# Performance work log

Measured on AMD Instinct MI355X. Metric: run time of the kernel, lower is better.

Reference implementation:

```python
import jax, jax.numpy as jnp
import numpy as np

C = 256
H = 4  # hard-coded head count in SA_Layer reshapes
EPS = 1e-5


def _bn(x, gamma, beta):
    # training-mode BatchNorm1d over (batch, length) per channel; x: [b,c,n]
    m = jnp.mean(x, axis=(0, 2), keepdims=True)
    v = jnp.var(x, axis=(0, 2), keepdims=True)
    return gamma[None, :, None] * (x - m) * jax.lax.rsqrt(v + EPS) + beta[None, :, None]


def _conv1(w, x, b=None):
    # 1x1 Conv1d == per-point matmul; w: [o,c], x: [b,c,n]
    y = jnp.einsum('oc,bcn->bon', w, x)
    return y if b is None else y + b[None, :, None]


def _sa_layer(x, xyz_emb, qk_w, v_w, v_b, t_w, t_b, bn_g, bn_b):
    b, c, n = x.shape
    h = x + xyz_emb                      # [b,c,n]
    q = _conv1(qk_w, h)                  # [b,c,n]  (q and k share weights)
    # quirky reshape: permute to [b,n,c] then view as [b,H,n,c//H]
    x_q = jnp.transpose(q, (0, 2, 1)).reshape(b, H, n, c // H)
    x_k = q.reshape(b, H, c // H, n)     # standard channel head split
    x_v = _conv1(v_w, h, v_b).reshape(b, H, c // H, n)
    energy = jnp.matmul(x_q, x_k)        # [b,H,n,n]
    att = jax.nn.softmax(energy, axis=-1)
    att = jax.nn.softmax(att, axis=-2)   # dual softmax
    x_r = jnp.matmul(x_v, att).reshape(b, c, n)
    x_r = jax.nn.relu(_bn(_conv1(t_w, x - x_r, t_b), bn_g, bn_b))
    return x + x_r


def setup_inputs() -> dict:
    key = jax.random.key(0)
    ks = jax.random.split(key, 16)
    B, N = 4, 2048
    s = 1.0 / np.sqrt(C)
    inp = {
        'x': jax.random.normal(ks[0], (B, C, N), jnp.float32),
        'xyz': jax.random.normal(ks[1], (B, N, 3), jnp.float32),
        'conv1_w': jax.random.normal(ks[2], (C, C), jnp.float32) * s,
        'pos_w': jax.random.normal(ks[3], (C, 3), jnp.float32) * 0.5,
        'pos_b': jax.random.normal(ks[4], (C,), jnp.float32) * 0.02,
        'bn1_g': jnp.ones((C,), jnp.float32),
        'bn1_b': jnp.zeros((C,), jnp.float32),
        'qk_w': jax.random.normal(ks[5], (4, C, C), jnp.float32) * s,
        'v_w': jax.random.normal(ks[6], (4, C, C), jnp.float32) * s,
        'v_b': jax.random.normal(ks[7], (4, C), jnp.float32) * 0.02,
        't_w': jax.random.normal(ks[8], (4, C, C), jnp.float32) * s,
        't_b': jax.random.normal(ks[9], (4, C), jnp.float32) * 0.02,
        'bn_g': jnp.ones((4, C), jnp.float32),
        'bn_b': jnp.zeros((4, C), jnp.float32),
    }
    return inp


def reference(x, xyz, conv1_w, pos_w, pos_b, bn1_g, bn1_b,
              qk_w, v_w, v_b, t_w, t_b, bn_g, bn_b):
    # xyz: [B,N,3] -> permute -> pos_xyz (1x1 conv)
    xyz_emb = jnp.einsum('oi,bni->bon', pos_w, xyz) + pos_b[None, :, None]  # [b,C,n]
    h = jax.nn.relu(_bn(_conv1(conv1_w, x), bn1_g, bn1_b))
    outs = []
    for i in range(4):
        h = _sa_layer(h, xyz_emb, qk_w[i], v_w[i], v_b[i],
                      t_w[i], t_b[i], bn_g[i], bn_b[i])
        outs.append(h)
    return jnp.concatenate(outs, axis=1)  # [b, 4*C, n]
```

## Files before the change

### kernel.cpp

```cpp
#include <hip/hip_runtime.h>
#include <math.h>

#define Bsz 4
#define Cch 256
#define Npt 2048
#define Hh  4
#define NL  4
#define BN_CNT (Bsz * Npt)
#define EPSV 1e-5f
#define NROW (16 * Npt)
#define L2E 1.44269504f

typedef _Float16 f16x8 __attribute__((ext_vector_type(8)));
typedef _Float16 f16x4 __attribute__((ext_vector_type(4)));
typedef float    f32x4 __attribute__((ext_vector_type(4)));

__device__ __forceinline__ float fexp2(float x) { return __builtin_amdgcn_exp2f(x); }

__device__ __forceinline__ void gld16(const _Float16* g, _Float16* l) {
    __builtin_amdgcn_global_load_lds(
        (const __attribute__((address_space(1))) unsigned int*)g,
        (__attribute__((address_space(3))) unsigned int*)l, 16, 0, 0);
}

__global__ void k_xyz_emb(const float* __restrict__ xyz, const float* __restrict__ pw,
                          const float* __restrict__ pb, float* __restrict__ emb) {
    int idx = blockIdx.x * 256 + threadIdx.x;
    int n = idx & (Npt - 1);
    int c = (idx >> 11) & (Cch - 1);
    int b = idx >> 19;
    const float* xz = xyz + (b * Npt + n) * 3;
    emb[idx] = pw[c * 3 + 0] * xz[0] + pw[c * 3 + 1] * xz[1] + pw[c * 3 + 2] * xz[2] + pb[c];
}

__global__ void k_castw(const float* __restrict__ c1w, const float* __restrict__ qkw,
                        const float* __restrict__ vw, const float* __restrict__ tw,
                        _Float16* __restrict__ o, float* __restrict__ bnacc) {
    int i = blockIdx.x * 256 + threadIdx.x;
    if (i < 5 * 512) bnacc[i] = 0.f;
    const float* src; int off;
    if (i < 65536)            { src = c1w; off = i; }
    else if (i < 327680)      { src = qkw; off = i - 65536; }
    else if (i < 589824)      { src = vw;  off = i - 327680; }
    else                      { src = tw;  off = i - 589824; }
    o[i] = (_Float16)src[off];
}

__global__ __launch_bounds__(256) void k_fuse_t(const float* __restrict__ in,
        _Float16* __restrict__ XT) {
    __shared__ _Float16 Tt[64][72];
    const int b = blockIdx.z, c0 = blockIdx.y * 64, n0 = blockIdx.x * 64;
    const int t = threadIdx.x;
    const int cl = t >> 2, ns = (t & 3) * 16;
    const float* ip = in + ((size_t)(b * Cch + c0 + cl) * Npt) + n0 + ns;
    #pragma unroll
    for (int g = 0; g < 4; ++g) {
        float4 v = *(const float4*)(ip + g * 4);
        Tt[ns + g * 4 + 0][cl] = (_Float16)v.x;
        Tt[ns + g * 4 + 1][cl] = (_Float16)v.y;
        Tt[ns + g * 4 + 2][cl] = (_Float16)v.z;
        Tt[ns + g * 4 + 3][cl] = (_Float16)v.w;
    }
    __syncthreads();
    int nl = t >> 2, cs = (t & 3) * 16;
    _Float16* op = XT + ((size_t)(b * Npt + n0 + nl) * Cch) + c0 + cs;
    #pragma unroll
    for (int g = 0; g < 4; ++g)
        *(f16x4*)(op + g * 4) = *(f16x4*)&Tt[nl][cs + g * 4];
}

__global__ __launch_bounds__(256) void k_gemm_mfma(const _Float16* __restrict__ Wb,
        const _Float16* __restrict__ XT, const float* __restrict__ bias,
        float* __restrict__ Yf, float* __restrict__ bnacc) {
    __shared__ float EpF[64][68];
    const int b = blockIdx.z, o0 = blockIdx.y * 64, n0 = blockIdx.x * 64;
    const int tid = threadIdx.x, w = tid >> 6, quad = (tid >> 4) & 3, tx = tid & 15;
    const _Float16* Arow = Wb + (o0 + w * 16 + tx) * Cch + quad * 8;
    const _Float16* Brow = XT + ((size_t)(b * Npt + n0 + tx) * Cch) + quad * 8;
    f32x4 acc[4];
    #pragma unroll
    for (int s = 0; s < 4; ++s) acc[s] = (f32x4){0.f, 0.f, 0.f, 0.f};
    for (int k0 = 0; k0 < Cch; k0 += 32) {
        f16x8 a = *(const f16x8*)(Arow + k0);
        #pragma unroll
        for (int s = 0; s < 4; ++s) {
            f16x8 bb = *(const f16x8*)(Brow + s * 16 * Cch + k0);
            acc[s] = __builtin_amdgcn_mfma_f32_16x16x32_f16(a, bb, acc[s], 0, 0, 0);
        }
    }
    float bv[4];
    {
        int ob = o0 + w * 16 + quad * 4;
        if (bias) { bv[0] = bias[ob]; bv[1] = bias[ob + 1]; bv[2] = bias[ob + 2]; bv[3] = bias[ob + 3]; }
        else bv[0] = bv[1] = bv[2] = bv[3] = 0.f;
    }
    #pragma unroll
    for (int s = 0; s < 4; ++s) {
        int ol = w * 16 + quad * 4, nl = s * 16 + tx;
        EpF[ol + 0][nl] = acc[s][0] + bv[0];
        EpF[ol + 1][nl] = acc[s][1] + bv[1];
        EpF[ol + 2][nl] = acc[s][2] + bv[2];
        EpF[ol + 3][nl] = acc[s][3] + bv[3];
    }
    __syncthreads();
    int row = tid >> 2, seg = (tid & 3) * 16;
    float* yp = Yf + ((size_t)(b * Cch + o0 + row) * Npt) + n0 + seg;
    float s1 = 0.f, s2 = 0.f;
    #pragma unroll
    for (int g = 0; g < 4; ++g) {
        float4 v = *(float4*)&EpF[row][seg + g * 4];
        *(float4*)(yp + g * 4) = v;
        s1 += v.x + v.y + v.z + v.w;
        s2 += v.x * v.x + v.y * v.y + v.z * v.z + v.w * v.w;
    }
    s1 += __shfl_xor(s1, 1); s2 += __shfl_xor(s2, 1);
    s1 += __shfl_xor(s1, 2); s2 += __shfl_xor(s2, 2);
    if ((tid & 3) == 0) {
        atomicAdd(&bnacc[o0 + row], s1);
        atomicAdd(&bnacc[256 + o0 + row], s2);
    }
}

__global__ __launch_bounds__(256) void k_gemm_qkv(const _Float16* __restrict__ Wqk,
        const _Float16* __restrict__ Wv, const _Float16* __restrict__ XT,
        const float* __restrict__ vbias, _Float16* __restrict__ Vb,
        _Float16* __restrict__ Qg, _Float16* __restrict__ Kt) {
    __shared__ _Float16 EpB[64][72];
    const int b = blockIdx.z, y = blockIdx.y, n0 = blockIdx.x * 64;
    const int isV = (y >= 4);
    const int o0 = (isV ? (y - 4) : y) * 64;
    const _Float16* Wb = isV ? Wv : Wqk;
    const int tid = threadIdx.x, w = tid >> 6, quad = (tid >> 4) & 3, tx = tid & 15;
    const _Float16* Arow = Wb + (o0 + w * 16 + tx) * Cch + quad * 8;
    const _Float16* Brow = XT + ((size_t)(b * Npt + n0 + tx) * Cch) + quad * 8;
    f32x4 acc[4];
    #pragma unroll
    for (int s = 0; s < 4; ++s) acc[s] = (f32x4){0.f, 0.f, 0.f, 0.f};
    for (int k0 = 0; k0 < Cch; k0 += 32) {
        f16x8 a = *(const f16x8*)(Arow + k0);
        #pragma unroll
        for (int s = 0; s < 4; ++s) {
            f16x8 bb = *(const f16x8*)(Brow + s * 16 * Cch + k0);
            acc[s] = __builtin_amdgcn_mfma_f32_16x16x32_f16(a, bb, acc[s], 0, 0, 0);
        }
    }
    if (!isV) {
        const int cch = (w << 1) + (quad >> 1);
        const int hof = (quad & 1) * 4;
        #pragma unroll
        for (int s = 0; s < 4; ++s) {
            int ng = n0 + s * 16 + tx;
            f16x4 pk;
            pk[0] = (_Float16)acc[s][0]; pk[1] = (_Float16)acc[s][1];
            pk[2] = (_Float16)acc[s][2]; pk[3] = (_Float16)acc[s][3];
            int rK = ng & 63, jt = ng >> 6;
            size_t ka = ((size_t)((b * Hh + (o0 >> 6)) * 32 + jt) << 12)
                      + rK * 64 + ((cch ^ (rK & 7)) * 8) + hof;
            *(f16x4*)&Kt[ka] = pk;
            int iQ = ((ng & 511) << 2) + (o0 >> 6);
            int rQ = iQ & 63, it = iQ >> 6;
            size_t qa = ((size_t)((b * Hh + (ng >> 9)) * 32 + it) << 12)
                      + rQ * 64 + ((cch ^ (rQ & 7)) * 8) + hof;
            *(f16x4*)&Qg[qa] = pk;
        }
        return;
    }
    float bv[4];
    {
        int ob = o0 + w * 16 + quad * 4;
        bv[0] = vbias[ob]; bv[1] = vbias[ob + 1]; bv[2] = vbias[ob + 2]; bv[3] = vbias[ob + 3];
    }
    #pragma unroll
    for (int s = 0; s < 4; ++s) {
        int ol = w * 16 + quad * 4, nl = s * 16 + tx;
        EpB[ol + 0][nl] = (_Float16)(acc[s][0] + bv[0]);
        EpB[ol + 1][nl] = (_Float16)(acc[s][1] + bv[1]);
        EpB[ol + 2][nl] = (_Float16)(acc[s][2] + bv[2]);
        EpB[ol + 3][nl] = (_Float16)(acc[s][3] + bv[3]);
    }
    __syncthreads();
    int row = tid >> 2, seg = (tid & 3) * 16;
    const int m = tid & 3;
    const int pbase = (m >> 1) * 32 + (m & 1) * 4;
    _Float16* yp = Vb + ((size_t)(b * Cch + o0 + row) * Npt) + n0 + pbase;
    #pragma unroll
    for (int g = 0; g < 4; ++g)
        *(f16x4*)(yp + g * 8) = *(f16x4*)&EpB[row][seg + g * 4];
}

__global__ __launch_bounds__(256) void k_attn_A(const _Float16* __restrict__ Qg,
        const _Float16* __restrict__ Kt, float* __restrict__ mP, float* __restrict__ lP) {
    __shared__ _Float16 Ksh[2][4096];
    const int flat = blockIdx.x;
    const int bh = (flat & 7) * 2 + ((flat >> 3) & 1);
    const int rest = flat >> 4;
    const int i0 = (rest & 15) * 128;
    const int jc = rest >> 4;
    const int tid = threadIdx.x, w = tid >> 6, q = (tid >> 4) & 3, tx = tid & 15;
    const int lane = tid & 63;
    const int sx = tx & 7;
    f16x8 qa[2][2];
    #pragma unroll
    for (int g = 0; g < 2; ++g) {
        const _Float16* Qtile = Qg + ((size_t)(bh * 32 + ((i0 + g * 64) >> 6)) << 12);
        int r = w * 16 + tx;
        qa[g][0] = *(const f16x8*)(Qtile + r * 64 + (q ^ sx) * 8);
        qa[g][1] = *(const f16x8*)(Qtile + r * 64 + ((q + 4) ^ sx) * 8);
    }
    const _Float16* Kbase = Kt + ((size_t)(bh * 32) << 12);
    const int jt0 = jc * 8;
    {
        const _Float16* g = Kbase + ((size_t)jt0 << 12) + (w * 2) * 512 + lane * 8;
        gld16(g,       &Ksh[0][(w * 2 + 0) * 512]);
        gld16(g + 512, &Ksh[0][(w * 2 + 1) * 512]);
    }
    __syncthreads();
    float m2[2][4], l[2][4];
    #pragma unroll
    for (int g = 0; g < 2; ++g)
        #pragma unroll
        for (int r = 0; r < 4; ++r) { m2[g][r] = -1e30f; l[g][r] = 0.f; }
    for (int t = 0; t < 8; ++t) {
        if (t < 7) {
            const _Float16* g = Kbase + ((size_t)(jt0 + t + 1) << 12) + (w * 2) * 512 + lane * 8;
            gld16(g,       &Ksh[(t + 1) & 1][(w * 2 + 0) * 512]);
            gld16(g + 512, &Ksh[(t + 1) & 1][(w * 2 + 1) * 512]);
        }
        const _Float16* kbuf = Ksh[t & 1];
        f32x4 e[2][4];
        #pragma unroll
        for (int s = 0; s < 4; ++s) {
            int r = s * 16 + tx;
            f16x8 kb0 = *(const f16x8*)(kbuf + r * 64 + (q ^ sx) * 8);
            f16x8 kb1 = *(const f16x8*)(kbuf + r * 64 + ((q + 4) ^ sx) * 8);
            #pragma unroll
            for (int g = 0; g < 2; ++g) {
                f32x4 z = (f32x4){0.f, 0.f, 0.f, 0.f};
                z = __builtin_amdgcn_mfma_f32_16x16x32_f16(qa[g][0], kb0, z, 0, 0, 0);
                e[g][s] = __builtin_amdgcn_mfma_f32_16x16x32_f16(qa[g][1], kb1, z, 0, 0, 0);
            }
        }
        #pragma unroll
        for (int g = 0; g < 2; ++g)
            #pragma unroll
            for (int r = 0; r < 4; ++r) {
                float e0 = e[g][0][r] * L2E, e1 = e[g][1][r] * L2E;
                float e2 = e[g][2][r] * L2E, e3 = e[g][3][r] * L2E;
                float lm = fmaxf(fmaxf(e0, e1), fmaxf(e2, e3));
                float nm = fmaxf(m2[g][r], lm);
                l[g][r] = l[g][r] * fexp2(m2[g][r] - nm)
                        + fexp2(e0 - nm) + fexp2(e1 - nm) + fexp2(e2 - nm) + fexp2(e3 - nm);
                m2[g][r] = nm;
            }
        __syncthreads();
    }
    #pragma unroll
    for (int g = 0; g < 2; ++g)
        #pragma unroll
        for (int r = 0; r < 4; ++r) {
            float mm = m2[g][r], ll = l[g][r];
            #pragma unroll
            for (int off = 1; off < 16; off <<= 1) {
                float om = __shfl_xor(mm, off), ol = __shfl_xor(ll, off);
                float nm = fmaxf(mm, om);
                ll = ll * fexp2(mm - nm) + ol * fexp2(om - nm);
                mm = nm;
            }
            if (tx == 0) {
                int idx = bh * Npt + i0 + g * 64 + w * 16 + q * 4 + r;
                mP[jc * NROW + idx] = mm;
                lP[jc * NROW + idx] = ll;
            }
        }
}

__global__ __launch_bounds__(256, 2) void k_attn_B(const _Float16* __restrict__ Qg,
        const _Float16* __restrict__ Kt, const _Float16* __restrict__ Vb,
        const float* __restrict__ mP, const float* __restrict__ lP,
        const float* __restrict__ h, _Float16* __restrict__ XT) {
    __shared__ float mlm[Npt];
    __shared__ float mll[Npt];
    __shared__ float Ssh[4][64];
    __shared__ _Float16 TS[4][4096];
    const int flat = blockIdx.x;
    const int bh = (flat & 7) * 2 + ((flat >> 3) & 1);
    const int j0 = (flat >> 4) * 64;
    const int b = bh >> 2, hd = bh & 3;
    const int tid = threadIdx.x, w = tid >> 6, q = (tid >> 4) & 3, tx = tid & 15;
    const int sx = tx & 7;
    {
        const int ib = tid * 8;
        #pragma unroll
        for (int e = 0; e < 2; ++e) {
            int ii = ib + e * 4;
            int idx = bh * Npt + ii;
            float4 m0 = *(const float4*)&mP[idx];
            float4 m1 = *(const float4*)&mP[NROW + idx];
            float4 m2 = *(const float4*)&mP[2 * NROW + idx];
            float4 m3 = *(const float4*)&mP[3 * NROW + idx];
            float4 l0 = *(const float4*)&lP[idx];
            float4 l1 = *(const float4*)&lP[NROW + idx];
            float4 l2 = *(const float4*)&lP[2 * NROW + idx];
            float4 l3 = *(const float4*)&lP[3 * NROW + idx];
            #pragma unroll
            for (int k = 0; k < 4; ++k) {
                float a0 = ((const float*)&m0)[k], a1 = ((const float*)&m1)[k];
                float a2 = ((const float*)&m2)[k], a3 = ((const float*)&m3)[k];
                float mm = fmaxf(fmaxf(a0, a1), fmaxf(a2, a3));
                float ll = ((const float*)&l0)[k] * fexp2(a0 - mm)
                         + ((const float*)&l1)[k] * fexp2(a1 - mm)
                         + ((const float*)&l2)[k] * fexp2(a2 - mm)
                         + ((const float*)&l3)[k] * fexp2(a3 - mm);
                mlm[ii + k] = mm;
                mll[ii + k] = L2E / ll;
            }
        }
    }
    f16x8 kb[4][2];
    {
        const _Float16* Ktile = Kt + ((size_t)(bh * 32 + (j0 >> 6)) << 12);
        #pragma unroll
        for (int nt = 0; nt < 4; ++nt) {
            int r = nt * 16 + tx;
            kb[nt][0] = *(const f16x8*)(Ktile + r * 64 + (q ^ sx) * 8);
            kb[nt][1] = *(const f16x8*)(Ktile + r * 64 + ((q + 4) ^ sx) * 8);
        }
    }
    __syncthreads();
    f32x4 Tacc[4][4];
    #pragma unroll
    for (int mt = 0; mt < 4; ++mt)
        #pragma unroll
        for (int nt = 0; nt < 4; ++nt) Tacc[mt][nt] = (f32x4){0.f, 0.f, 0.f, 0.f};
    float scS[4] = {0.f, 0.f, 0.f, 0.f};
    const _Float16* vbase = Vb + (size_t)(b * Cch + hd * 64) * Npt;
    for (int it = 0; it < 8; ++it) {
        const int i0 = w * 512 + it * 64;
        const _Float16* Qtile = Qg + ((size_t)(bh * 32 + (i0 >> 6)) << 12);
        #pragma unroll
        for (int pp = 0; pp < 2; ++pp) {
            f16x4 pk[2][4];
            #pragma unroll
            for (int mt2 = 0; mt2 < 2; ++mt2) {
                const int mt = pp * 2 + mt2;
                const int r = mt * 16 + tx;
                f16x8 qa0 = *(const f16x8*)(Qtile + r * 64 + (q ^ sx) * 8);
                f16x8 qa1 = *(const f16x8*)(Qtile + r * 64 + ((q + 4) ^ sx) * 8);
                float4 m2v = *(const float4*)&mlm[i0 + mt * 16 + q * 4];
                float4 liv = *(const float4*)&mll[i0 + mt * 16 + q * 4];
                #pragma unroll
                for (int nt = 0; nt < 4; ++nt) {
                    f32x4 z = (f32x4){0.f, 0.f, 0.f, 0.f};
                    z = __builtin_amdgcn_mfma_f32_16x16x32_f16(qa0, kb[nt][0], z, 0, 0, 0);
                    z = __builtin_amdgcn_mfma_f32_16x16x32_f16(qa1, kb[nt][1], z, 0, 0, 0);
                    float a0 = fexp2(fexp2(__builtin_fmaf(z[0], L2E, -m2v.x)) * liv.x);
                    float a1 = fexp2(fexp2(__builtin_fmaf(z[1], L2E, -m2v.y)) * liv.y);
                    float a2 = fexp2(fexp2(__builtin_fmaf(z[2], L2E, -m2v.z)) * liv.z);
                    float a3 = fexp2(fexp2(__builtin_fmaf(z[3], L2E, -m2v.w)) * liv.w);
                    scS[nt] += a0 + a1 + a2 + a3;
                    f16x4 pkk;
                    pkk[0] = (_Float16)a0; pkk[1] = (_Float16)a1;
                    pkk[2] = (_Float16)a2; pkk[3] = (_Float16)a3;
                    pk[mt2][nt] = pkk;
                }
            }
            #pragma unroll
            for (int mtd = 0; mtd < 4; ++mtd) {
                f16x8 va = *(const f16x8*)(vbase + (size_t)(mtd * 16 + tx) * Npt + i0 + pp * 32 + q * 8);
                #pragma unroll
                for (int nt = 0; nt < 4; ++nt) {
                    f16x8 pb = __builtin_shufflevector(pk[0][nt], pk[1][nt], 0, 1, 2, 3, 4, 5, 6, 7);
                    Tacc[mtd][nt] = __builtin_amdgcn_mfma_f32_16x16x32_f16(va, pb, Tacc[mtd][nt], 0, 0, 0);
                }
            }
        }
    }
    #pragma unroll
    for (int nt = 0; nt < 4; ++nt) {
        float s = scS[nt];
        s += __shfl_xor(s, 16);
        s += __shfl_xor(s, 32);
        if (q == 0) Ssh[w][nt * 16 + tx] = s;
    }
    #pragma unroll
    for (int mtd = 0; mtd < 4; ++mtd)
        #pragma unroll
        for (int nt = 0; nt < 4; ++nt) {
            f16x4 pkk;
            pkk[0] = (_Float16)Tacc[mtd][nt][0];
            pkk[1] = (_Float16)Tacc[mtd][nt][1];
            pkk[2] = (_Float16)Tacc[mtd][nt][2];
            pkk[3] = (_Float16)Tacc[mtd][nt][3];
            *(f16x4*)&TS[w][(nt * 16 + tx) * 64 + ((2 * mtd + (q >> 1)) ^ sx) * 8 + (q & 1) * 4] = pkk;
        }
    __syncthreads();
    {
        const int jl = tid >> 2, d4 = tid & 3;
        const float s4 = Ssh[0][jl] + Ssh[1][jl] + Ssh[2][jl] + Ssh[3][jl];
        const float rs = 1.f / s4;
        const int jg = j0 + jl;
        #pragma unroll
        for (int g = 0; g < 2; ++g) {
            const int s8 = d4 * 2 + g;
            const int base = jl * 64 + ((s8 ^ (jl & 7)) * 8);
            f16x8 t0 = *(const f16x8*)&TS[0][base];
            f16x8 t1 = *(const f16x8*)&TS[1][base];
            f16x8 t2 = *(const f16x8*)&TS[2][base];
            f16x8 t3 = *(const f16x8*)&TS[3][base];
            const float* hp = h + ((size_t)(b * Cch + hd * 64 + s8 * 8) * Npt) + jg;
            f16x8 u;
            #pragma unroll
            for (int e = 0; e < 8; ++e) {
                float tv = (float)t0[e] + (float)t1[e] + (float)t2[e] + (float)t3[e];
                u[e] = (_Float16)(hp[(size_t)e * Npt] - tv * rs);
            }
            *(f16x8*)(XT + ((size_t)(b * Npt + jg) * Cch) + hd * 64 + s8 * 8) = u;
        }
    }
}

__global__ __launch_bounds__(256) void k_bn_fuse(const float* __restrict__ t,
        const float* __restrict__ bnacc,
        const float* __restrict__ g, const float* __restrict__ bt,
        const float* __restrict__ emb, const float* __restrict__ resid,
        float* __restrict__ hout, float* __restrict__ out, _Float16* __restrict__ XT,
        int layer) {
    __shared__ _Float16 Tt[64][72];
    const int b = blockIdx.z, c0 = blockIdx.y * 64, n0 = blockIdx.x * 64;
    const int tt = threadIdx.x;
    const int cl = tt >> 2, ns = (tt & 3) * 16;
    const int c = c0 + cl;
    const float mn = bnacc[c] * (1.f / BN_CNT);
    const float var = bnacc[256 + c] * (1.f / BN_CNT) - mn * mn;
    const float is = rsqrtf(var + EPSV);
    const float gg = g[c], bb = bt[c];
    const size_t rowoff = ((size_t)(b * Cch + c) * Npt) + n0 + ns;
    const float* tp = t + rowoff;
    const float* ep = emb + rowoff;
    const float* rp = resid ? resid + rowoff : nullptr;
    float* hp = hout + rowoff;
    float* op = out ? out + (size_t)b * (NL * Cch * Npt) + (size_t)(layer * Cch + c) * Npt + n0 + ns
                    : nullptr;
    #pragma unroll
    for (int gi = 0; gi < 4; ++gi) {
        float4 v = *(const float4*)(tp + gi * 4);
        float4 y;
        y.x = fmaxf(gg * (v.x - mn) * is + bb, 0.f);
        y.y = fmaxf(gg * (v.y - mn) * is + bb, 0.f);
        y.z = fmaxf(gg * (v.z - mn) * is + bb, 0.f);
        y.w = fmaxf(gg * (v.w - mn) * is + bb, 0.f);
        if (rp) {
            float4 r = *(const float4*)(rp + gi * 4);
            y.x += r.x; y.y += r.y; y.z += r.z; y.w += r.w;
        }
        *(float4*)(hp + gi * 4) = y;
        if (op) *(float4*)(op + gi * 4) = y;
        float4 e = *(const float4*)(ep + gi * 4);
        Tt[ns + gi * 4 + 0][cl] = (_Float16)(y.x + e.x);
        Tt[ns + gi * 4 + 1][cl] = (_Float16)(y.y + e.y);
        Tt[ns + gi * 4 + 2][cl] = (_Float16)(y.z + e.z);
        Tt[ns + gi * 4 + 3][cl] = (_Float16)(y.w + e.w);
    }
    __syncthreads();
    int nl = tt >> 2, cs = (tt & 3) * 16;
    _Float16* xp = XT + ((size_t)(b * Npt + n0 + nl) * Cch) + c0 + cs;
    #pragma unroll
    for (int gi = 0; gi < 4; ++gi)
        *(f16x4*)(xp + gi * 4) = *(f16x4*)&Tt[nl][cs + gi * 4];
}

extern "C" void kernel_launch(void* const* d_in, const int* in_sizes, int n_in,
                              void* d_out, int out_size, void* d_ws, size_t ws_size,
                              hipStream_t stream) {
    (void)in_sizes; (void)n_in; (void)out_size; (void)ws_size;
    const float* x    = (const float*)d_in[0];
    const float* xyz  = (const float*)d_in[1];
    const float* c1w  = (const float*)d_in[2];
    const float* posw = (const float*)d_in[3];
    const float* posb = (const float*)d_in[4];
    const float* bn1g = (const float*)d_in[5];
    const float* bn1b = (const float*)d_in[6];
    const float* qkw  = (const float*)d_in[7];
    const float* vw   = (const float*)d_in[8];
    const float* vb   = (const float*)d_in[9];
    const float* tw   = (const float*)d_in[10];
    const float* tb   = (const float*)d_in[11];
    const float* bng  = (const float*)d_in[12];
    const float* bnb  = (const float*)d_in[13];
    float* out = (float*)d_out;

    const size_t NE = (size_t)Bsz * Cch * Npt;
    char* W = (char*)d_ws;
    float* emb   = (float*)W;                 W += NE * 4;
    float* h     = (float*)W;                 W += NE * 4;
    float* vbuf  = (float*)W;                 W += NE * 4;
    _Float16* XT = (_Float16*)W;              W += NE * 2;
    _Float16* Qg = (_Float16*)W;              W += NE * 2;
    _Float16* Kt = (_Float16*)W;              W += NE * 2;
    _Float16* Vb = (_Float16*)W;              W += NE * 2;
    _Float16* wbf = (_Float16*)W;             W += 851968 * 2;
    float* mP    = (float*)W;                 W += 4 * NROW * 4;
    float* lP    = (float*)W;                 W += 4 * NROW * 4;
    float* bnacc = (float*)W;                 W += 5 * 512 * 4;

    dim3 blk(256);
    dim3 g4(Npt / 64, Cch / 64, Bsz);
    dim3 gQKV(Npt / 64, 8, Bsz);
    int ew = (int)(NE / 256);

    k_castw<<<3328, blk, 0, stream>>>(c1w, qkw, vw, tw, wbf, bnacc);
    k_xyz_emb<<<ew, blk, 0, stream>>>(xyz, posw, posb, emb);

    k_fuse_t<<<g4, blk, 0, stream>>>(x, XT);
    k_gemm_mfma<<<g4, blk, 0, stream>>>(wbf, XT, nullptr, vbuf, bnacc);
    k_bn_fuse<<<g4, blk, 0, stream>>>(vbuf, bnacc, bn1g, bn1b, emb, nullptr,
                                      h, nullptr, XT, 0);

    for (int L = 0; L < NL; ++L) {
        const _Float16* qkL = wbf + 65536 + (size_t)L * 65536;
        const _Float16* vL  = wbf + 327680 + (size_t)L * 65536;
        const _Float16* tL  = wbf + 589824 + (size_t)L * 65536;
        float* accL = bnacc + (1 + L) * 512;
        k_gemm_qkv<<<gQKV, blk, 0, stream>>>(qkL, vL, XT, vb + L * Cch, Vb, Qg, Kt);
        k_attn_A<<<1024, blk, 0, stream>>>(Qg, Kt, mP, lP);
        k_attn_B<<<512, blk, 0, stream>>>(Qg, Kt, Vb, mP, lP, h, XT);
        k_gemm_mfma<<<g4, blk, 0, stream>>>(tL, XT, tb + L * Cch, vbuf, accL);
        k_bn_fuse<<<g4, blk, 0, stream>>>(vbuf, accL, bng + L * Cch, bnb + L * Cch,
                                          emb, h, h, out, XT, L);
    }
}
```

Baseline: 558.6 us.

## Load K directly from global in attn_A and hoist Q/V loads in attn_B

In k_attn_A, the double-buffered LDS staging of K tiles via global_load_lds is replaced by direct per-thread global loads into registers. This drops the shared-memory buffer and the per-tile __syncthreads, and a launch bound of 3 blocks per SM is set to favour occupancy. In the second attention kernel, Q and V fragments for an iteration are loaded up front, and s_setprio is wrapped around the MFMA bursts to overlap memory latency with compute. The trade-offs are higher register pressure and reliance on cache for K reuse across waves, since each wave now fetches K itself.

```diff
diff --git a/kernel.cpp b/kernel.cpp
--- a/kernel.cpp
+++ b/kernel.cpp
@@ -16,12 +16,6 @@
 typedef float    f32x4 __attribute__((ext_vector_type(4)));
 
 __device__ __forceinline__ float fexp2(float x) { return __builtin_amdgcn_exp2f(x); }
-
-__device__ __forceinline__ void gld16(const _Float16* g, _Float16* l) {
-    __builtin_amdgcn_global_load_lds(
-        (const __attribute__((address_space(1))) unsigned int*)g,
-        (__attribute__((address_space(3))) unsigned int*)l, 16, 0, 0);
-}
 
 __global__ void k_xyz_emb(const float* __restrict__ xyz, const float* __restrict__ pw,
                           const float* __restrict__ pb, float* __restrict__ emb) {
@@ -188,16 +182,14 @@
         *(f16x4*)(yp + g * 8) = *(f16x4*)&EpB[row][seg + g * 4];
 }
 
-__global__ __launch_bounds__(256) void k_attn_A(const _Float16* __restrict__ Qg,
+__global__ __launch_bounds__(256, 3) void k_attn_A(const _Float16* __restrict__ Qg,
         const _Float16* __restrict__ Kt, float* __restrict__ mP, float* __restrict__ lP) {
-    __shared__ _Float16 Ksh[2][4096];
     const int flat = blockIdx.x;
     const int bh = (flat & 7) * 2 + ((flat >> 3) & 1);
     const int rest = flat >> 4;
     const int i0 = (rest & 15) * 128;
     const int jc = rest >> 4;
     const int tid = threadIdx.x, w = tid >> 6, q = (tid >> 4) & 3, tx = tid & 15;
-    const int lane = tid & 63;
     const int sx = tx & 7;
     f16x8 qa[2][2];
     #pragma unroll
@@ -209,50 +201,42 @@
     }
     const _Float16* Kbase = Kt + ((size_t)(bh * 32) << 12);
     const int jt0 = jc * 8;
-    {
-        const _Float16* g = Kbase + ((size_t)jt0 << 12) + (w * 2) * 512 + lane * 8;
-        gld16(g,       &Ksh[0][(w * 2 + 0) * 512]);
-        gld16(g + 512, &Ksh[0][(w * 2 + 1) * 512]);
-    }
-    __syncthreads();
     float m2[2][4], l[2][4];
     #pragma unroll
     for (int g = 0; g < 2; ++g)
         #pragma unroll
         for (int r = 0; r < 4; ++r) { m2[g][r] = -1e30f; l[g][r] = 0.f; }
     for (int t = 0; t < 8; ++t) {
-        if (t < 7) {
-            const _Float16* g = Kbase + ((size_t)(jt0 + t + 1) << 12) + (w * 2) * 512 + lane * 8;
-            gld16(g,       &Ksh[(t + 1) & 1][(w * 2 + 0) * 512]);
-            gld16(g + 512, &Ksh[(t + 1) & 1][(w * 2 + 1) * 512]);
-        }
-        const _Float16* kbuf = Ksh[t & 1];
-        f32x4 e[2][4];
+        const _Float16* kpage = Kbase + ((size_t)(jt0 + t) << 12);
+        f16x8 kb0[4], kb1[4];
         #pragma unroll
         for (int s = 0; s < 4; ++s) {
             int r = s * 16 + tx;
-            f16x8 kb0 = *(const f16x8*)(kbuf + r * 64 + (q ^ sx) * 8);
-            f16x8 kb1 = *(const f16x8*)(kbuf + r * 64 + ((q + 4) ^ sx) * 8);
-            #pragma unroll
-            for (int g = 0; g < 2; ++g) {
+            kb0[s] = *(const f16x8*)(kpage + r * 64 + (q ^ sx) * 8);
+            kb1[s] = *(const f16x8*)(kpage + r * 64 + ((q + 4) ^ sx) * 8);
+        }
+        #pragma unroll
+        for (int g = 0; g < 2; ++g) {
+            f32x4 e[4];
+            __builtin_amdgcn_s_setprio(1);
+            #pragma unroll
+            for (int s = 0; s < 4; ++s) {
                 f32x4 z = (f32x4){0.f, 0.f, 0.f, 0.f};
-                z = __builtin_amdgcn_mfma_f32_16x16x32_f16(qa[g][0], kb0, z, 0, 0, 0);
-                e[g][s] = __builtin_amdgcn_mfma_f32_16x16x32_f16(qa[g][1], kb1, z, 0, 0, 0);
-            }
-        }
-        #pragma unroll
-        for (int g = 0; g < 2; ++g)
+                z = __builtin_amdgcn_mfma_f32_16x16x32_f16(qa[g][0], kb0[s], z, 0, 0, 0);
+                e[s] = __builtin_amdgcn_mfma_f32_16x16x32_f16(qa[g][1], kb1[s], z, 0, 0, 0);
+            }
+            __builtin_amdgcn_s_setprio(0);
             #pragma unroll
             for (int r = 0; r < 4; ++r) {
-                float e0 = e[g][0][r] * L2E, e1 = e[g][1][r] * L2E;
-                float e2 = e[g][2][r] * L2E, e3 = e[g][3][r] * L2E;
+                float e0 = e[0][r] * L2E, e1 = e[1][r] * L2E;
+                float e2 = e[2][r] * L2E, e3 = e[3][r] * L2E;
                 float lm = fmaxf(fmaxf(e0, e1), fmaxf(e2, e3));
                 float nm = fmaxf(m2[g][r], lm);
                 l[g][r] = l[g][r] * fexp2(m2[g][r] - nm)
                         + fexp2(e0 - nm) + fexp2(e1 - nm) + fexp2(e2 - nm) + fexp2(e3 - nm);
                 m2[g][r] = nm;
             }
-        __syncthreads();
+        }
     }
     #pragma unroll
     for (int g = 0; g < 2; ++g)
@@ -337,22 +321,33 @@
     for (int it = 0; it < 8; ++it) {
         const int i0 = w * 512 + it * 64;
         const _Float16* Qtile = Qg + ((size_t)(bh * 32 + (i0 >> 6)) << 12);
+        f16x8 qv[2][2][2];
+        f16x8 vv[2][4];
+        #pragma unroll
+        for (int pp = 0; pp < 2; ++pp) {
+            #pragma unroll
+            for (int mt2 = 0; mt2 < 2; ++mt2) {
+                const int r = (pp * 2 + mt2) * 16 + tx;
+                qv[pp][mt2][0] = *(const f16x8*)(Qtile + r * 64 + (q ^ sx) * 8);
+                qv[pp][mt2][1] = *(const f16x8*)(Qtile + r * 64 + ((q + 4) ^ sx) * 8);
+            }
+            #pragma unroll
+            for (int mtd = 0; mtd < 4; ++mtd)
+                vv[pp][mtd] = *(const f16x8*)(vbase + (size_t)(mtd * 16 + tx) * Npt + i0 + pp * 32 + q * 8);
+        }
         #pragma unroll
         for (int pp = 0; pp < 2; ++pp) {
             f16x4 pk[2][4];
             #pragma unroll
             for (int mt2 = 0; mt2 < 2; ++mt2) {
                 const int mt = pp * 2 + mt2;
-                const int r = mt * 16 + tx;
-                f16x8 qa0 = *(const f16x8*)(Qtile + r * 64 + (q ^ sx) * 8);
-                f16x8 qa1 = *(const f16x8*)(Qtile + r * 64 + ((q + 4) ^ sx) * 8);
                 float4 m2v = *(const float4*)&mlm[i0 + mt * 16 + q * 4];
                 float4 liv = *(const float4*)&mll[i0 + mt * 16 + q * 4];
                 #pragma unroll
                 for (int nt = 0; nt < 4; ++nt) {
                     f32x4 z = (f32x4){0.f, 0.f, 0.f, 0.f};
-                    z = __builtin_amdgcn_mfma_f32_16x16x32_f16(qa0, kb[nt][0], z, 0, 0, 0);
-                    z = __builtin_amdgcn_mfma_f32_16x16x32_f16(qa1, kb[nt][1], z, 0, 0, 0);
+                    z = __builtin_amdgcn_mfma_f32_16x16x32_f16(qv[pp][mt2][0], kb[nt][0], z, 0, 0, 0);
+                    z = __builtin_amdgcn_mfma_f32_16x16x32_f16(qv[pp][mt2][1], kb[nt][1], z, 0, 0, 0);
                     float a0 = fexp2(fexp2(__builtin_fmaf(z[0], L2E, -m2v.x)) * liv.x);
                     float a1 = fexp2(fexp2(__builtin_fmaf(z[1], L2E, -m2v.y)) * liv.y);
                     float a2 = fexp2(fexp2(__builtin_fmaf(z[2], L2E, -m2v.z)) * liv.z);
@@ -364,15 +359,16 @@
                     pk[mt2][nt] = pkk;
                 }
             }
+            __builtin_amdgcn_s_setprio(1);
             #pragma unroll
             for (int mtd = 0; mtd < 4; ++mtd) {
-                f16x8 va = *(const f16x8*)(vbase + (size_t)(mtd * 16 + tx) * Npt + i0 + pp * 32 + q * 8);
                 #pragma unroll
                 for (int nt = 0; nt < 4; ++nt) {
                     f16x8 pb = __builtin_shufflevector(pk[0][nt], pk[1][nt], 0, 1, 2, 3, 4, 5, 6, 7);
-                    Tacc[mtd][nt] = __builtin_amdgcn_mfma_f32_16x16x32_f16(va, pb, Tacc[mtd][nt], 0, 0, 0);
+                    Tacc[mtd][nt] = __builtin_amdgcn_mfma_f32_16x16x32_f16(vv[pp][mtd], pb, Tacc[mtd][nt], 0, 0, 0);
                 }
             }
+            __builtin_amdgcn_s_setprio(0);
         }
     }
     #pragma unroll
```

Result: no change. 550.6 us (-1.4%).
